# Performance work log

Measured on AMD Instinct MI355X. Metric: run time of the kernel, lower is better.

Reference implementation:

```python
import jax, jax.numpy as jnp
import numpy as np
import math

D = 256
N = 2048
B = 8
N_PLUS_1 = 2048  # masked index (1-based) in the score matrix


def setup_inputs() -> dict:
    key = jax.random.key(0)
    k1, k2, k3, k4, k5 = jax.random.split(key, 5)
    scale = 1.0 / math.sqrt(D)
    return {
        "Z_in": jax.random.normal(k1, (B, D + 1, N), dtype=jnp.float32),
        "A_l": jax.random.normal(k2, (D, D), dtype=jnp.float32) * scale,
        "r_l": jax.random.normal(k3, (1,), dtype=jnp.float32),
        "B_l": jax.random.normal(k4, (D, D), dtype=jnp.float32) * scale,
        "C_l": jax.random.normal(k5, (D, D), dtype=jnp.float32) * scale,
    }


def reference(Z_in, A_l, r_l, B_l, C_l):
    # Z_in: (B, d+1, N)
    X = Z_in[:, :D, :]   # (B, d, N)
    Y = Z_in[:, D:, :]   # (B, 1, N)
    U = jnp.einsum('ij,bjn->bin', B_l, X)  # (B, d, N)
    W = jnp.einsum('ij,bjn->bin', C_l, X)  # (B, d, N)
    scores = jnp.einsum('bdn,bdm->bnm', U, W)  # (B, N, N) = U^T W
    att = jax.nn.relu(scores)                  # h_type == 'relu'
    # zero the (n_plus_1-1, n_plus_1-1) diagonal entry of the attention core
    att = att.at[:, N_PLUS_1 - 1, N_PLUS_1 - 1].set(0.0)
    X_att = jnp.einsum('bdn,bnm->bdm', X, att)  # (B, d, N)
    X_out = X + jnp.einsum('ij,bjm->bim', A_l, X_att)
    Y_out = Y + r_l * jnp.einsum('bdn,bnm->bdm', Y, att)
    return jnp.concatenate([X_out, Y_out], axis=1)  # (B, d+1, N)
```

## Files before the change

kernel.cpp:

```cpp
#include <hip/hip_runtime.h>

#define D 256
#define N 2048
#define NB 8
#define ZSTRIDE (257 * 2048)

typedef __attribute__((ext_vector_type(8))) short short8;
typedef __attribute__((ext_vector_type(4))) short short4v;
typedef __attribute__((ext_vector_type(4))) float f32x4;

#define MFMA(a, b, c) __builtin_amdgcn_mfma_f32_16x16x32_bf16((a), (b), (c), 0, 0, 0)

#define GLOAD_LDS16(g, s) __builtin_amdgcn_global_load_lds( \
    (const __attribute__((address_space(1))) void*)(g),     \
    (__attribute__((address_space(3))) void*)(s), 16, 0, 0)

__device__ __forceinline__ short f2bf(float f) {
    unsigned u = __builtin_bit_cast(unsigned, f);
    u += 0x7fffu + ((u >> 16) & 1u);
    return (short)(u >> 16);
}
__device__ __forceinline__ float bf2f(short s) {
    unsigned u = ((unsigned)(unsigned short)s) << 16;
    return __builtin_bit_cast(float, u);
}

__global__ __launch_bounds__(256) void prep_small(
    const float* __restrict__ B_l, const float* __restrict__ C_l,
    const float* __restrict__ A_l, const float* __restrict__ Z,
    short* __restrict__ G, short* __restrict__ Ab, short* __restrict__ Yb)
{
    int blk = blockIdx.x, tid = threadIdx.x;
    if (blk < 256) {
        float s = 0.f;
        #pragma unroll 8
        for (int k = 0; k < 256; ++k)
            s += B_l[k * 256 + blk] * C_l[k * 256 + tid];
        G[blk * 256 + tid] = f2bf(s);
    } else if (blk < 320) {
        int base = (blk - 256) * 1024 + tid;
        #pragma unroll
        for (int r = 0; r < 4; ++r) {
            int idx = base + r * 256;
            Ab[idx] = f2bf(A_l[idx]);
        }
    } else {
        int base = (blk - 320) * 1024 + tid;
        #pragma unroll
        for (int r = 0; r < 4; ++r) {
            int idx = base + r * 256;
            int b = idx >> 11, n = idx & 2047;
            Yb[idx] = f2bf(Z[(size_t)b * ZSTRIDE + 256 * N + n]);
        }
    }
}

__global__ __launch_bounds__(256) void transpose_kernel(
    const float* __restrict__ Z, short* __restrict__ Xt)
{
    typedef __attribute__((ext_vector_type(4))) float f4;
    __shared__ short t[64][68];
    int blk = blockIdx.x;
    int b = blk & 7;
    int dt = (blk >> 3) & 3;
    int nt = blk >> 5;
    int d0 = dt * 64, n0 = nt * 64;
    const float* ZB = Z + (size_t)b * ZSTRIDE;
    int tid = threadIdx.x;
    #pragma unroll
    for (int k = 0; k < 4; ++k) {
        int f = tid + k * 256;
        int r = f >> 4, c4 = f & 15;
        f4 v = *(const f4*)(ZB + (size_t)(d0 + r) * N + n0 + c4 * 4);
        #pragma unroll
        for (int j = 0; j < 4; ++j) t[r][c4 * 4 + j] = f2bf(v[j]);
    }
    __syncthreads();
    short* XtB = Xt + (size_t)b * (N * D);
    #pragma unroll
    for (int k = 0; k < 2; ++k) {
        int f = tid + k * 256;
        int n = f >> 3, c8 = f & 7;
        short8 v;
        #pragma unroll
        for (int j = 0; j < 8; ++j) v[j] = t[c8 * 8 + j][n];
        *(short8*)(XtB + (size_t)(n0 + n) * D + d0 + c8 * 8) = v;
    }
}

__global__ __launch_bounds__(512, 4) void prep_gemm2(
    const short* __restrict__ Xt, const short* __restrict__ G,
    const short* __restrict__ Ab, short* __restrict__ Wt, short* __restrict__ Px)
{
    __shared__ __align__(16) char smem[65536];
    typedef short TileT[128][64];
    TileT* As = (TileT*)smem;
    TileT* Bs = (TileT*)(smem + 32768);

    int blk = blockIdx.x;
    int half = blk >> 8;
    int r0 = blk & 255;
    int b = r0 >> 5;
    int idx = r0 & 31;

    const short* Arows;
    const short* Brows;
    short* Cout;
    size_t cstride;
    int row_base, col_base;
    if (half == 0) {
        row_base = (idx & 15) << 7;
        col_base = (idx >> 4) << 7;
        Arows = Xt + (size_t)b * (N * D);
        Brows = G;
        Cout  = Wt + (size_t)b * (N * D);
        cstride = D;
    } else {
        row_base = (idx & 1) << 7;
        col_base = (idx >> 1) << 7;
        Arows = Ab;
        Brows = Xt + (size_t)b * (N * D);
        Cout  = Px + (size_t)b * (D * N);
        cstride = N;
    }

    int tid = threadIdx.x;
    int w = tid >> 6, l = tid & 63;
    int l16 = l & 15, lq = l >> 4;
    int wm = w >> 2, wn = w & 3;
    int lrow8 = l >> 3, lc = l & 7;

    auto STAGE = [&](const short* base, int row0g, int kt, TileT* dst) {
        #pragma unroll
        for (int i = 0; i < 2; ++i) {
            int rloc = i * 64 + w * 8;
            int row = rloc + lrow8;
            const char* src = (const char*)(base + (size_t)(row0g + row) * D)
                              + kt * 128 + ((lc ^ (row & 7)) * 16);
            GLOAD_LDS16(src, &(*dst)[rloc][0]);
        }
    };

    f32x4 zero4 = {0.f, 0.f, 0.f, 0.f};
    f32x4 acc[4][2];
    #pragma unroll
    for (int mi = 0; mi < 4; ++mi)
        #pragma unroll
        for (int ni = 0; ni < 2; ++ni) acc[mi][ni] = zero4;

    STAGE(Arows, row_base, 0, &As[0]);
    STAGE(Brows, col_base, 0, &Bs[0]);
    __syncthreads();

    int buf = 0;
    #pragma unroll
    for (int kt = 0; kt < 4; ++kt) {
        if (kt < 3) {
            STAGE(Arows, row_base, kt + 1, &As[buf ^ 1]);
            STAGE(Brows, col_base, kt + 1, &Bs[buf ^ 1]);
        }
        #pragma unroll
        for (int ks = 0; ks < 2; ++ks) {
            short8 af[4], bf[2];
            #pragma unroll
            for (int mi = 0; mi < 4; ++mi) {
                int r = wm * 64 + mi * 16 + l16;
                af[mi] = *(const short8*)(&As[buf][r][(ks * 32 + lq * 8) ^ ((r & 7) << 3)]);
            }
            #pragma unroll
            for (int ni = 0; ni < 2; ++ni) {
                int r = wn * 32 + ni * 16 + l16;
                bf[ni] = *(const short8*)(&Bs[buf][r][(ks * 32 + lq * 8) ^ ((r & 7) << 3)]);
            }
            #pragma unroll
            for (int mi = 0; mi < 4; ++mi)
                #pragma unroll
                for (int ni = 0; ni < 2; ++ni)
                    acc[mi][ni] = MFMA(af[mi], bf[ni], acc[mi][ni]);
        }
        __syncthreads();
        buf ^= 1;
    }

    short* cq = (short*)smem + (size_t)w * (64 * 40);
    #pragma unroll
    for (int mi = 0; mi < 4; ++mi)
        #pragma unroll
        for (int ni = 0; ni < 2; ++ni)
            #pragma unroll
            for (int rg = 0; rg < 4; ++rg)
                cq[(mi * 16 + lq * 4 + rg) * 40 + ni * 16 + l16] =
                    f2bf(acc[mi][ni][rg]);
    #pragma unroll
    for (int p = 0; p < 4; ++p) {
        int row = p * 16 + (l >> 2), c8 = l & 3;
        short8 v = *(const short8*)(&cq[row * 40 + c8 * 8]);
        *(short8*)(Cout + (size_t)(row_base + wm * 64 + row) * cstride +
                   col_base + wn * 32 + c8 * 8) = v;
    }
}

__global__ __launch_bounds__(512, 4) void scores_kernel(
    const short* __restrict__ Xt, const short* __restrict__ Wt,
    const short* __restrict__ Yb, short* __restrict__ attT,
    float* __restrict__ accY, int bBase, int nbMask, int nbShift)
{
    __shared__ __align__(16) char smem[65536];
    typedef short TileT[128][64];
    TileT* As = (TileT*)smem;
    TileT* Bs = (TileT*)(smem + 32768);

    int blk = blockIdx.x;
    int b_local = blk & nbMask;
    int idx = blk >> nbShift;
    int m_base = (idx & 15) << 7;
    int n_base = (idx >> 4) << 7;
    int b = bBase + b_local;

    int tid = threadIdx.x;
    int w = tid >> 6, l = tid & 63;
    int l16 = l & 15, lq = l >> 4;
    int wm = w >> 2, wn = w & 3;
    int lrow8 = l >> 3, lc = l & 7;

    const short* WtB = Wt + (size_t)b * (N * D);
    const short* XtB = Xt + (size_t)b * (N * D);
    const short* YbB = Yb + (size_t)b * N;
    float* accYB = accY + (size_t)b * N;
    short* attTB = attT + (size_t)b_local * N * N;

    auto STAGE = [&](const short* base, int row0g, int kt, TileT* dst) {
        #pragma unroll
        for (int i = 0; i < 2; ++i) {
            int rloc = i * 64 + w * 8;
            int row = rloc + lrow8;
            const char* src = (const char*)(base + (size_t)(row0g + row) * D)
                              + kt * 128 + ((lc ^ (row & 7)) * 16);
            GLOAD_LDS16(src, &(*dst)[rloc][0]);
        }
    };

    f32x4 zero4 = {0.f, 0.f, 0.f, 0.f};
    f32x4 acc[4][2];
    #pragma unroll
    for (int mi = 0; mi < 4; ++mi)
        #pragma unroll
        for (int ni = 0; ni < 2; ++ni) acc[mi][ni] = zero4;

    STAGE(WtB, m_base, 0, &As[0]);
    STAGE(XtB, n_base, 0, &Bs[0]);
    __syncthreads();

    int buf = 0;
    #pragma unroll
    for (int kt = 0; kt < 4; ++kt) {
        if (kt < 3) {
            STAGE(WtB, m_base, kt + 1, &As[buf ^ 1]);
            STAGE(XtB, n_base, kt + 1, &Bs[buf ^ 1]);
        }
        #pragma unroll
        for (int ks = 0; ks < 2; ++ks) {
            short8 af[4], bf[2];
            #pragma unroll
            for (int mi = 0; mi < 4; ++mi) {
                int r = wm * 64 + mi * 16 + l16;
                af[mi] = *(const short8*)(&As[buf][r][(ks * 32 + lq * 8) ^ ((r & 7) << 3)]);
            }
            #pragma unroll
            for (int ni = 0; ni < 2; ++ni) {
                int r = wn * 32 + ni * 16 + l16;
                bf[ni] = *(const short8*)(&Bs[buf][r][(ks * 32 + lq * 8) ^ ((r & 7) << 3)]);
            }
            #pragma unroll
            for (int mi = 0; mi < 4; ++mi)
                #pragma unroll
                for (int ni = 0; ni < 2; ++ni)
                    acc[mi][ni] = MFMA(af[mi], bf[ni], acc[mi][ni]);
        }
        __syncthreads();
        buf ^= 1;
    }

    bool corner = (m_base == 1920) && (n_base == 1920);
    #pragma unroll
    for (int mi = 0; mi < 4; ++mi)
        #pragma unroll
        for (int ni = 0; ni < 2; ++ni)
            #pragma unroll
            for (int rg = 0; rg < 4; ++rg) {
                float v = acc[mi][ni][rg];
                v = v > 0.f ? v : 0.f;
                if (corner) {
                    int gm = m_base + wm * 64 + mi * 16 + lq * 4 + rg;
                    int gn = n_base + wn * 32 + ni * 16 + l16;
                    if (gm == N - 1 && gn == N - 1) v = 0.f;
                }
                acc[mi][ni][rg] = v;
            }

    {
        float yv[2];
        #pragma unroll
        for (int ni = 0; ni < 2; ++ni)
            yv[ni] = bf2f(YbB[n_base + wn * 32 + ni * 16 + l16]);
        #pragma unroll
        for (int mi = 0; mi < 4; ++mi)
            #pragma unroll
            for (int rg = 0; rg < 4; ++rg) {
                float s = acc[mi][0][rg] * yv[0] + acc[mi][1][rg] * yv[1];
                s += __shfl_xor(s, 1);
                s += __shfl_xor(s, 2);
                s += __shfl_xor(s, 4);
                s += __shfl_xor(s, 8);
                if (l16 == 0)
                    atomicAdd(&accYB[m_base + wm * 64 + mi * 16 + lq * 4 + rg], s);
            }
    }

    {
        short* attq = (short*)smem + (size_t)w * (64 * 40);
        #pragma unroll
        for (int mi = 0; mi < 4; ++mi)
            #pragma unroll
            for (int ni = 0; ni < 2; ++ni)
                #pragma unroll
                for (int rg = 0; rg < 4; ++rg)
                    attq[(mi * 16 + lq * 4 + rg) * 40 + ni * 16 + l16] =
                        f2bf(acc[mi][ni][rg]);
        #pragma unroll
        for (int p = 0; p < 4; ++p) {
            int row = p * 16 + (l >> 2), c8 = l & 3;
            short8 v = *(const short8*)(&attq[row * 40 + c8 * 8]);
            *(short8*)(attTB + (size_t)(m_base + wm * 64 + row) * N +
                       n_base + wn * 32 + c8 * 8) = v;
        }
    }
}

__global__ __launch_bounds__(512, 4) void pv_kernel(
    const float* __restrict__ Z, const short* __restrict__ Px,
    const short* __restrict__ attT, float* __restrict__ out,
    int bBase, int nbMask, int nbShift)
{
    __shared__ __align__(16) char smem[49152];
    typedef short ATile[64][64];
    typedef short BTile[128][64];
    ATile* As = (ATile*)smem;
    BTile* Bs = (BTile*)(smem + 16384);

    int blk = blockIdx.x;
    int b_local = blk & nbMask;
    int idx = blk >> nbShift;
    int d_base = (idx & 3) << 6;
    int m_base = (idx >> 2) << 7;
    int b = bBase + b_local;

    int tid = threadIdx.x;
    int w = tid >> 6, l = tid & 63;
    int l16 = l & 15, lq = l >> 4;
    int wd = w >> 2, wm = w & 3;
    int lrow8 = l >> 3, lc = l & 7;

    const short* PxB = Px + (size_t)b * (D * N);
    const short* attTB = attT + (size_t)b_local * N * N;

    auto STAGE_A = [&](int kt, ATile* dst) {
        int rloc = w * 8;
        int row = rloc + lrow8;
        const char* src = (const char*)(PxB + (size_t)(d_base + row) * N)
                          + kt * 128 + ((lc ^ (row & 7)) * 16);
        GLOAD_LDS16(src, &(*dst)[rloc][0]);
    };
    auto STAGE_B = [&](int kt, BTile* dst) {
        #pragma unroll
        for (int i = 0; i < 2; ++i) {
            int rloc = i * 64 + w * 8;
            int row = rloc + lrow8;
            const char* src = (const char*)(attTB + (size_t)(m_base + row) * N)
                              + kt * 128 + ((lc ^ (row & 7)) * 16);
            GLOAD_LDS16(src, &(*dst)[rloc][0]);
        }
    };

    f32x4 zero4 = {0.f, 0.f, 0.f, 0.f};
    f32x4 acc[2][2];
    #pragma unroll
    for (int di = 0; di < 2; ++di)
        #pragma unroll
        for (int mj = 0; mj < 2; ++mj) acc[di][mj] = zero4;

    STAGE_A(0, &As[0]);
    STAGE_B(0, &Bs[0]);
    __syncthreads();

    int buf = 0;
    for (int kt = 0; kt < 32; ++kt) {
        if (kt < 31) {
            STAGE_A(kt + 1, &As[buf ^ 1]);
            STAGE_B(kt + 1, &Bs[buf ^ 1]);
        }
        #pragma unroll
        for (int ks = 0; ks < 2; ++ks) {
            short8 af[2], bf[2];
            #pragma unroll
            for (int di = 0; di < 2; ++di) {
                int r = wd * 32 + di * 16 + l16;
                af[di] = *(const short8*)(&As[buf][r][(ks * 32 + lq * 8) ^ ((r & 7) << 3)]);
            }
            #pragma unroll
            for (int mj = 0; mj < 2; ++mj) {
                int r = wm * 32 + mj * 16 + l16;
                bf[mj] = *(const short8*)(&Bs[buf][r][(ks * 32 + lq * 8) ^ ((r & 7) << 3)]);
            }
            #pragma unroll
            for (int di = 0; di < 2; ++di)
                #pragma unroll
                for (int mj = 0; mj < 2; ++mj)
                    acc[di][mj] = MFMA(af[di], bf[mj], acc[di][mj]);
        }
        __syncthreads();
        buf ^= 1;
    }

    #pragma unroll
    for (int di = 0; di < 2; ++di)
        #pragma unroll
        for (int mj = 0; mj < 2; ++mj)
            #pragma unroll
            for (int rg = 0; rg < 4; ++rg) {
                int dd = d_base + wd * 32 + di * 16 + lq * 4 + rg;
                int mm = m_base + wm * 32 + mj * 16 + l16;
                size_t off = (size_t)b * ZSTRIDE + (size_t)dd * N + mm;
                out[off] = Z[off] + acc[di][mj][rg];
            }
}

__global__ __launch_bounds__(256) void epilogue_y(
    const float* __restrict__ Z, const float* __restrict__ accY,
    const float* __restrict__ r_l, float* __restrict__ out)
{
    int i = blockIdx.x * 256 + threadIdx.x;
    int b = i >> 11, m = i & 2047;
    size_t off = (size_t)b * ZSTRIDE + (size_t)256 * N + m;
    out[off] = Z[off] + r_l[0] * accY[i];
}

__global__ __launch_bounds__(512, 4) void fused_kernel(
    const float* __restrict__ Z, const short* __restrict__ Xt,
    const short* __restrict__ Wt, const short* __restrict__ Px,
    const short* __restrict__ Yb, const float* __restrict__ r_l,
    float* __restrict__ out)
{
    __shared__ __align__(16) short xtsA[32][256];
    __shared__ __align__(16) short xtsB[32][256];
    __shared__ __align__(16) short attA[64][36];
    __shared__ __align__(16) short attB[64][36];

    int blk = blockIdx.x;
    int b = blk & 7;
    int m_base = (blk >> 3) << 6;
    int tid = threadIdx.x;
    int w = tid >> 6, l = tid & 63;
    int l16 = l & 15, lq = l >> 4;

    const short* XtB = Xt + (size_t)b * (N * D);
    const short* WtB = Wt + (size_t)b * (N * D);
    const short* PxB = Px + (size_t)b * (D * N);
    const short* YbB = Yb + b * N;

    int mi = w >> 1;
    int nj = w & 1;

    short8 a_wt[8];
    {
        const short* ap = WtB + (size_t)(m_base + 16 * mi + l16) * D + lq * 8;
        #pragma unroll
        for (int ks = 0; ks < 8; ++ks)
            a_wt[ks] = *(const short8*)(ap + ks * 32);
    }

    f32x4 zero4 = {0.f, 0.f, 0.f, 0.f};
    f32x4 accX[2][4];
    #pragma unroll
    for (int di = 0; di < 2; ++di)
        #pragma unroll
        for (int mj = 0; mj < 4; ++mj) accX[di][mj] = zero4;

    float accY = 0.f;
    int ym = tid >> 3, yseg = tid & 7;

    auto STAGE = [&](int it, short (*dst)[256]) {
        #pragma unroll
        for (int r = 0; r < 2; ++r) {
            int row  = r * 16 + 2 * w + (l >> 5);
            int colb = ((l & 31) * 16) ^ ((row & 7) << 4);
            const char* src = (const char*)(XtB + (size_t)(it * 32 + row) * D) + colb;
            GLOAD_LDS16(src, &dst[r * 16 + 2 * w][0]);
        }
    };

    auto BODY = [&](int it, short (*xrd)[256], short (*xst)[256], short (*atw)[36]) {
        int n_base = it * 32;
        if (it + 1 < 64) STAGE(it + 1, xst);
        short8 px[2];
        #pragma unroll
        for (int di = 0; di < 2; ++di)
            px[di] = *(const short8*)(PxB + (size_t)(32 * w + 16 * di + l16) * N +
                                      n_base + lq * 8);
        short4v yv = *(const short4v*)(YbB + n_base + yseg * 4);
        f32x4 sa = zero4;
        #pragma unroll
        for (int ks = 0; ks < 8; ++ks) {
            int colsh = (ks * 32 + lq * 8) ^ ((l16 & 7) << 3);
            short8 xb = *(const short8*)(&xrd[16 * nj + l16][colsh]);
            sa = MFMA(a_wt[ks], xb, sa);
        }
        {
            int nn = 16 * nj + l16;
            #pragma unroll
            for (int rg = 0; rg < 4; ++rg) {
                int mm = 16 * mi + lq * 4 + rg;
                float v = sa[rg] > 0.f ? sa[rg] : 0.f;
                if ((m_base + mm == N - 1) && (n_base + nn == N - 1)) v = 0.f;
                atw[mm][nn] = f2bf(v);
            }
        }
        __syncthreads();
        #pragma unroll
        for (int mj = 0; mj < 4; ++mj) {
            short8 bfr = *(const short8*)(&atw[16 * mj + l16][lq * 8]);
            #pragma unroll
            for (int di = 0; di < 2; ++di)
                accX[di][mj] = MFMA(px[di], bfr, accX[di][mj]);
        }
        {
            short4v av = *(const short4v*)(&atw[ym][yseg * 4]);
            #pragma unroll
            for (int j = 0; j < 4; ++j)
                accY += bf2f(av[j]) * bf2f(yv[j]);
        }
    };

    STAGE(0, xtsA);
    __syncthreads();
    for (int it2 = 0; it2 < 32; ++it2) {
        BODY(2 * it2,     xtsA, xtsB, attA);
        BODY(2 * it2 + 1, xtsB, xtsA, attB);
    }

    #pragma unroll
    for (int di = 0; di < 2; ++di)
        #pragma unroll
        for (int mj = 0; mj < 4; ++mj)
            #pragma unroll
            for (int rg = 0; rg < 4; ++rg) {
                int dd = 32 * w + 16 * di + lq * 4 + rg;
                int mm = m_base + 16 * mj + l16;
                size_t off = (size_t)b * ZSTRIDE + (size_t)dd * N + mm;
                out[off] = Z[off] + accX[di][mj][rg];
            }
    accY += __shfl_xor(accY, 1);
    accY += __shfl_xor(accY, 2);
    accY += __shfl_xor(accY, 4);
    if (yseg == 0) {
        float r = r_l[0];
        int mm = m_base + ym;
        size_t off = (size_t)b * ZSTRIDE + (size_t)256 * N + mm;
        out[off] = Z[off] + r * accY;
    }
}

extern "C" void kernel_launch(void* const* d_in, const int* in_sizes, int n_in,
                              void* d_out, int out_size, void* d_ws, size_t ws_size,
                              hipStream_t stream) {
    const float* Z   = (const float*)d_in[0];
    const float* A_l = (const float*)d_in[1];
    const float* r_l = (const float*)d_in[2];
    const float* B_l = (const float*)d_in[3];
    const float* C_l = (const float*)d_in[4];
    float* out = (float*)d_out;

    char* ws = (char*)d_ws;
    short* G    = (short*)(ws);
    short* Ab   = (short*)(ws + 131072);
    short* Xt   = (short*)(ws + 262144);
    short* Wt   = (short*)(ws + 8650752);
    short* Px   = (short*)(ws + 17039360);
    short* Yb   = (short*)(ws + 25427968);
    float* accY = (float*)(ws + 25460736);
    short* attT = (short*)(ws + 25526272);

    const size_t baseNeed = 25526272;
    const size_t attSz = (size_t)N * N * 2;
    int NBCH = 8, nbShift = 3;
    while (NBCH > 1 && baseNeed + (size_t)NBCH * attSz > ws_size) { NBCH >>= 1; --nbShift; }
    bool decomposed = (baseNeed + (size_t)NBCH * attSz <= ws_size);

    prep_small<<<336, 256, 0, stream>>>(B_l, C_l, A_l, Z, G, Ab, Yb);
    transpose_kernel<<<1024, 256, 0, stream>>>(Z, Xt);
    prep_gemm2<<<512, 512, 0, stream>>>(Xt, G, Ab, Wt, Px);

    if (decomposed) {
        hipMemsetAsync(accY, 0, NB * N * sizeof(float), stream);
        int nbMask = NBCH - 1;
        for (int c = 0; c < NB / NBCH; ++c) {
            int bBase = c * NBCH;
            scores_kernel<<<NBCH * 256, 512, 0, stream>>>(
                Xt, Wt, Yb, attT, accY, bBase, nbMask, nbShift);
            pv_kernel<<<NBCH * 64, 512, 0, stream>>>(
                Z, Px, attT, out, bBase, nbMask, nbShift);
        }
        epilogue_y<<<64, 256, 0, stream>>>(Z, accY, r_l, out);
    } else {
        fused_kernel<<<256, 512, 0, stream>>>(Z, Xt, Wt, Px, Yb, r_l, out);
    }
}
```

Measured before the change: 103.0 us.

## Keep Wt fragments in registers across eight N-tiles and enlarge pv tiles

The scores kernel now loads each wave's Wt row fragments into registers once, then loops over eight consecutive 128-column N tiles, streaming only Xt through double-buffered LDS and writing each output tile in turn. This removes the repeated staging of Wt and cuts the grid from 256 to 32 blocks per batch. The pv kernel doubles its M tile to 256, so each wave holds more accumulators and each A tile is reused across more columns. In exchange, register pressure rises (launch bounds relaxed to 2), LDS use grows, and fewer blocks may leave some CUs underoccupied.

```diff
diff --git a/kernel.cpp b/kernel.cpp
--- a/kernel.cpp
+++ b/kernel.cpp
@@ -200,21 +200,19 @@
     }
 }
 
-__global__ __launch_bounds__(512, 4) void scores_kernel(
+__global__ __launch_bounds__(512, 2) void scores_kernel(
     const short* __restrict__ Xt, const short* __restrict__ Wt,
     const short* __restrict__ Yb, short* __restrict__ attT,
     float* __restrict__ accY, int bBase, int nbMask, int nbShift)
 {
-    __shared__ __align__(16) char smem[65536];
-    typedef short TileT[128][64];
-    TileT* As = (TileT*)smem;
-    TileT* Bs = (TileT*)(smem + 32768);
+    __shared__ __align__(16) short Bs[2][128][64];
+    __shared__ __align__(16) short scratch[8][64][40];
 
     int blk = blockIdx.x;
     int b_local = blk & nbMask;
     int idx = blk >> nbShift;
     int m_base = (idx & 15) << 7;
-    int n_base = (idx >> 4) << 7;
+    int nsup = (idx >> 4) << 10;
     int b = bBase + b_local;
 
     int tid = threadIdx.x;
@@ -229,110 +227,123 @@
     float* accYB = accY + (size_t)b * N;
     short* attTB = attT + (size_t)b_local * N * N;
 
-    auto STAGE = [&](const short* base, int row0g, int kt, TileT* dst) {
+    short8 af[4][4][2];
+    #pragma unroll
+    for (int mi = 0; mi < 4; ++mi)
+        #pragma unroll
+        for (int kt = 0; kt < 4; ++kt)
+            #pragma unroll
+            for (int ks = 0; ks < 2; ++ks)
+                af[mi][kt][ks] = *(const short8*)(
+                    WtB + (size_t)(m_base + wm * 64 + mi * 16 + l16) * D +
+                    kt * 64 + ks * 32 + lq * 8);
+
+    f32x4 zero4 = {0.f, 0.f, 0.f, 0.f};
+    f32x4 acc[4][2];
+    #pragma unroll
+    for (int mi = 0; mi < 4; ++mi)
+        #pragma unroll
+        for (int ni = 0; ni < 2; ++ni) acc[mi][ni] = zero4;
+
+    auto STAGE_B = [&](int nb, int kt, int bufidx) {
         #pragma unroll
         for (int i = 0; i < 2; ++i) {
             int rloc = i * 64 + w * 8;
             int row = rloc + lrow8;
-            const char* src = (const char*)(base + (size_t)(row0g + row) * D)
+            const char* src = (const char*)(XtB + (size_t)(nb + row) * D)
                               + kt * 128 + ((lc ^ (row & 7)) * 16);
-            GLOAD_LDS16(src, &(*dst)[rloc][0]);
+            GLOAD_LDS16(src, &Bs[bufidx][rloc][0]);
         }
     };
 
-    f32x4 zero4 = {0.f, 0.f, 0.f, 0.f};
-    f32x4 acc[4][2];
-    #pragma unroll
-    for (int mi = 0; mi < 4; ++mi)
-        #pragma unroll
-        for (int ni = 0; ni < 2; ++ni) acc[mi][ni] = zero4;
-
-    STAGE(WtB, m_base, 0, &As[0]);
-    STAGE(XtB, n_base, 0, &Bs[0]);
+    STAGE_B(nsup, 0, 0);
     __syncthreads();
 
-    int buf = 0;
-    #pragma unroll
-    for (int kt = 0; kt < 4; ++kt) {
-        if (kt < 3) {
-            STAGE(WtB, m_base, kt + 1, &As[buf ^ 1]);
-            STAGE(XtB, n_base, kt + 1, &Bs[buf ^ 1]);
-        }
-        #pragma unroll
-        for (int ks = 0; ks < 2; ++ks) {
-            short8 af[4], bf[2];
-            #pragma unroll
-            for (int mi = 0; mi < 4; ++mi) {
-                int r = wm * 64 + mi * 16 + l16;
-                af[mi] = *(const short8*)(&As[buf][r][(ks * 32 + lq * 8) ^ ((r & 7) << 3)]);
-            }
-            #pragma unroll
-            for (int ni = 0; ni < 2; ++ni) {
-                int r = wn * 32 + ni * 16 + l16;
-                bf[ni] = *(const short8*)(&Bs[buf][r][(ks * 32 + lq * 8) ^ ((r & 7) << 3)]);
-            }
-            #pragma unroll
-            for (int mi = 0; mi < 4; ++mi)
+    for (int s = 0; s < 8; ++s) {
+        int n_base = nsup + s * 128;
+        #pragma unroll
+        for (int kt = 0; kt < 4; ++kt) {
+            if (kt < 3) {
+                STAGE_B(n_base, kt + 1, (kt + 1) & 1);
+            } else if (s < 7) {
+                STAGE_B(n_base + 128, 0, 0);
+            }
+
+            #pragma unroll
+            for (int ks = 0; ks < 2; ++ks) {
+                short8 bf[2];
                 #pragma unroll
-                for (int ni = 0; ni < 2; ++ni)
-                    acc[mi][ni] = MFMA(af[mi], bf[ni], acc[mi][ni]);
-        }
-        __syncthreads();
-        buf ^= 1;
-    }
-
-    bool corner = (m_base == 1920) && (n_base == 1920);
-    #pragma unroll
-    for (int mi = 0; mi < 4; ++mi)
-        #pragma unroll
-        for (int ni = 0; ni < 2; ++ni)
-            #pragma unroll
-            for (int rg = 0; rg < 4; ++rg) {
-                float v = acc[mi][ni][rg];
-                v = v > 0.f ? v : 0.f;
-                if (corner) {
-                    int gm = m_base + wm * 64 + mi * 16 + lq * 4 + rg;
-                    int gn = n_base + wn * 32 + ni * 16 + l16;
-                    if (gm == N - 1 && gn == N - 1) v = 0.f;
+                for (int ni = 0; ni < 2; ++ni) {
+                    int r = wn * 32 + ni * 16 + l16;
+                    bf[ni] = *(const short8*)(
+                        &Bs[kt & 1][r][(ks * 32 + lq * 8) ^ ((r & 7) << 3)]);
                 }
-                acc[mi][ni][rg] = v;
-            }
-
-    {
-        float yv[2];
-        #pragma unroll
-        for (int ni = 0; ni < 2; ++ni)
-            yv[ni] = bf2f(YbB[n_base + wn * 32 + ni * 16 + l16]);
-        #pragma unroll
-        for (int mi = 0; mi < 4; ++mi)
-            #pragma unroll
-            for (int rg = 0; rg < 4; ++rg) {
-                float s = acc[mi][0][rg] * yv[0] + acc[mi][1][rg] * yv[1];
-                s += __shfl_xor(s, 1);
-                s += __shfl_xor(s, 2);
-                s += __shfl_xor(s, 4);
-                s += __shfl_xor(s, 8);
-                if (l16 == 0)
-                    atomicAdd(&accYB[m_base + wm * 64 + mi * 16 + lq * 4 + rg], s);
-            }
-    }
-
-    {
-        short* attq = (short*)smem + (size_t)w * (64 * 40);
-        #pragma unroll
-        for (int mi = 0; mi < 4; ++mi)
-            #pragma unroll
-            for (int ni = 0; ni < 2; ++ni)
                 #pragma unroll
-                for (int rg = 0; rg < 4; ++rg)
-                    attq[(mi * 16 + lq * 4 + rg) * 40 + ni * 16 + l16] =
-                        f2bf(acc[mi][ni][rg]);
-        #pragma unroll
-        for (int p = 0; p < 4; ++p) {
-            int row = p * 16 + (l >> 2), c8 = l & 3;
-            short8 v = *(const short8*)(&attq[row * 40 + c8 * 8]);
-            *(short8*)(attTB + (size_t)(m_base + wm * 64 + row) * N +
-                       n_base + wn * 32 + c8 * 8) = v;
+                for (int mi = 0; mi < 4; ++mi)
+                    #pragma unroll
+                    for (int ni = 0; ni < 2; ++ni)
+                        acc[mi][ni] = MFMA(af[mi][kt][ks], bf[ni], acc[mi][ni]);
+            }
+
+            if (kt == 3) {
+                bool corner = (m_base == 1920) && (n_base == 1920);
+                #pragma unroll
+                for (int mi = 0; mi < 4; ++mi)
+                    #pragma unroll
+                    for (int ni = 0; ni < 2; ++ni)
+                        #pragma unroll
+                        for (int rg = 0; rg < 4; ++rg) {
+                            float v = acc[mi][ni][rg];
+                            v = v > 0.f ? v : 0.f;
+                            if (corner) {
+                                int gm = m_base + wm * 64 + mi * 16 + lq * 4 + rg;
+                                int gn = n_base + wn * 32 + ni * 16 + l16;
+                                if (gm == N - 1 && gn == N - 1) v = 0.f;
+                            }
+                            acc[mi][ni][rg] = v;
+                        }
+                {
+                    float yv[2];
+                    #pragma unroll
+                    for (int ni = 0; ni < 2; ++ni)
+                        yv[ni] = bf2f(YbB[n_base + wn * 32 + ni * 16 + l16]);
+                    #pragma unroll
+                    for (int mi = 0; mi < 4; ++mi)
+                        #pragma unroll
+                        for (int rg = 0; rg < 4; ++rg) {
+                            float sY = acc[mi][0][rg] * yv[0] + acc[mi][1][rg] * yv[1];
+                            sY += __shfl_xor(sY, 1);
+                            sY += __shfl_xor(sY, 2);
+                            sY += __shfl_xor(sY, 4);
+                            sY += __shfl_xor(sY, 8);
+                            if (l16 == 0)
+                                atomicAdd(&accYB[m_base + wm * 64 + mi * 16 + lq * 4 + rg], sY);
+                        }
+                }
+                {
+                    short* sq = &scratch[w][0][0];
+                    #pragma unroll
+                    for (int mi = 0; mi < 4; ++mi)
+                        #pragma unroll
+                        for (int ni = 0; ni < 2; ++ni)
+                            #pragma unroll
+                            for (int rg = 0; rg < 4; ++rg)
+                                sq[(mi * 16 + lq * 4 + rg) * 40 + ni * 16 + l16] =
+                                    f2bf(acc[mi][ni][rg]);
+                    #pragma unroll
+                    for (int p = 0; p < 4; ++p) {
+                        int row = p * 16 + (l >> 2), c8 = l & 3;
+                        short8 v = *(const short8*)(&sq[row * 40 + c8 * 8]);
+                        *(short8*)(attTB + (size_t)(m_base + wm * 64 + row) * N +
+                                   n_base + wn * 32 + c8 * 8) = v;
+                    }
+                }
+                #pragma unroll
+                for (int mi = 0; mi < 4; ++mi)
+                    #pragma unroll
+                    for (int ni = 0; ni < 2; ++ni) acc[mi][ni] = zero4;
+            }
+            __syncthreads();
         }
     }
 }
@@ -342,9 +353,9 @@
     const short* __restrict__ attT, float* __restrict__ out,
     int bBase, int nbMask, int nbShift)
 {
-    __shared__ __align__(16) char smem[49152];
+    __shared__ __align__(16) char smem[81920];
     typedef short ATile[64][64];
-    typedef short BTile[128][64];
+    typedef short BTile[256][64];
     ATile* As = (ATile*)smem;
     BTile* Bs = (BTile*)(smem + 16384);
 
@@ -352,7 +363,7 @@
     int b_local = blk & nbMask;
     int idx = blk >> nbShift;
     int d_base = (idx & 3) << 6;
-    int m_base = (idx >> 2) << 7;
+    int m_base = (idx >> 2) << 8;
     int b = bBase + b_local;
 
     int tid = threadIdx.x;
@@ -373,7 +384,7 @@
     };
     auto STAGE_B = [&](int kt, BTile* dst) {
         #pragma unroll
-        for (int i = 0; i < 2; ++i) {
+        for (int i = 0; i < 4; ++i) {
             int rloc = i * 64 + w * 8;
             int row = rloc + lrow8;
             const char* src = (const char*)(attTB + (size_t)(m_base + row) * N)
@@ -383,11 +394,11 @@
     };
 
     f32x4 zero4 = {0.f, 0.f, 0.f, 0.f};
-    f32x4 acc[2][2];
+    f32x4 acc[2][4];
     #pragma unroll
     for (int di = 0; di < 2; ++di)
         #pragma unroll
-        for (int mj = 0; mj < 2; ++mj) acc[di][mj] = zero4;
+        for (int mj = 0; mj < 4; ++mj) acc[di][mj] = zero4;
 
     STAGE_A(0, &As[0]);
     STAGE_B(0, &Bs[0]);
@@ -401,21 +412,21 @@
         }
         #pragma unroll
         for (int ks = 0; ks < 2; ++ks) {
-            short8 af[2], bf[2];
+            short8 af[2], bf[4];
             #pragma unroll
             for (int di = 0; di < 2; ++di) {
                 int r = wd * 32 + di * 16 + l16;
                 af[di] = *(const short8*)(&As[buf][r][(ks * 32 + lq * 8) ^ ((r & 7) << 3)]);
             }
             #pragma unroll
-            for (int mj = 0; mj < 2; ++mj) {
-                int r = wm * 32 + mj * 16 + l16;
+            for (int mj = 0; mj < 4; ++mj) {
+                int r = wm * 64 + mj * 16 + l16;
                 bf[mj] = *(const short8*)(&Bs[buf][r][(ks * 32 + lq * 8) ^ ((r & 7) << 3)]);
             }
             #pragma unroll
             for (int di = 0; di < 2; ++di)
                 #pragma unroll
-                for (int mj = 0; mj < 2; ++mj)
+                for (int mj = 0; mj < 4; ++mj)
                     acc[di][mj] = MFMA(af[di], bf[mj], acc[di][mj]);
         }
         __syncthreads();
@@ -425,11 +436,11 @@
     #pragma unroll
     for (int di = 0; di < 2; ++di)
         #pragma unroll
-        for (int mj = 0; mj < 2; ++mj)
+        for (int mj = 0; mj < 4; ++mj)
             #pragma unroll
             for (int rg = 0; rg < 4; ++rg) {
                 int dd = d_base + wd * 32 + di * 16 + lq * 4 + rg;
-                int mm = m_base + wm * 32 + mj * 16 + l16;
+                int mm = m_base + wm * 64 + mj * 16 + l16;
                 size_t off = (size_t)b * ZSTRIDE + (size_t)dd * N + mm;
                 out[off] = Z[off] + acc[di][mj][rg];
             }
@@ -605,9 +616,9 @@
         int nbMask = NBCH - 1;
         for (int c = 0; c < NB / NBCH; ++c) {
             int bBase = c * NBCH;
-            scores_kernel<<<NBCH * 256, 512, 0, stream>>>(
+            scores_kernel<<<NBCH * 32, 512, 0, stream>>>(
                 Xt, Wt, Yb, attT, accY, bBase, nbMask, nbShift);
-            pv_kernel<<<NBCH * 64, 512, 0, stream>>>(
+            pv_kernel<<<NBCH * 32, 512, 0, stream>>>(
                 Z, Px, attT, out, bBase, nbMask, nbShift);
         }
         epilogue_y<<<64, 256, 0, stream>>>(Z, accY, r_l, out);
```

Result: slower. 120.1 us (+16.6%).

## Enlarge scores kernel tile to 128x256 with 32-wide K steps

Applied to the files above, without the earlier changes.

Changes the scores GEMM tile from 128x128 to 128x256 per block, so each wave computes 64x64 instead of 64x32. The K tile shrinks from 64 to 32 and the loop now runs 8 stages, with a new XOR swizzle for the narrower rows. The goal is more MFMA reuse per LDS fragment load and half as many blocks reloading the shared W rows. In exchange it uses more accumulator registers and synchronizes more often, and the grid halves, which lowers parallelism.

```diff
diff --git a/kernel.cpp b/kernel.cpp
--- a/kernel.cpp
+++ b/kernel.cpp
@@ -205,23 +205,24 @@
     const short* __restrict__ Yb, short* __restrict__ attT,
     float* __restrict__ accY, int bBase, int nbMask, int nbShift)
 {
-    __shared__ __align__(16) char smem[65536];
-    typedef short TileT[128][64];
-    TileT* As = (TileT*)smem;
-    TileT* Bs = (TileT*)(smem + 32768);
+    __shared__ __align__(16) char smem[49152];
+    typedef short ATile[128][32];
+    typedef short BTile[256][32];
+    ATile* As = (ATile*)smem;
+    BTile* Bs = (BTile*)(smem + 16384);
 
     int blk = blockIdx.x;
     int b_local = blk & nbMask;
     int idx = blk >> nbShift;
     int m_base = (idx & 15) << 7;
-    int n_base = (idx >> 4) << 7;
+    int n_base = (idx >> 4) << 8;
     int b = bBase + b_local;
 
     int tid = threadIdx.x;
     int w = tid >> 6, l = tid & 63;
     int l16 = l & 15, lq = l >> 4;
     int wm = w >> 2, wn = w & 3;
-    int lrow8 = l >> 3, lc = l & 7;
+    int lr4 = l >> 2, lc4 = l & 3;
 
     const short* WtB = Wt + (size_t)b * (N * D);
     const short* XtB = Xt + (size_t)b * (N * D);
@@ -229,85 +230,86 @@
     float* accYB = accY + (size_t)b * N;
     short* attTB = attT + (size_t)b_local * N * N;
 
-    auto STAGE = [&](const short* base, int row0g, int kt, TileT* dst) {
+    auto STAGE_A = [&](int kt, int bi) {
+        int row = w * 16 + lr4;
+        const char* src = (const char*)(WtB + (size_t)(m_base + row) * D)
+                          + kt * 64 + ((lc4 ^ ((row >> 1) & 3)) * 16);
+        GLOAD_LDS16(src, &As[bi][w * 16][0]);
+    };
+    auto STAGE_B = [&](int kt, int bi) {
         #pragma unroll
         for (int i = 0; i < 2; ++i) {
-            int rloc = i * 64 + w * 8;
-            int row = rloc + lrow8;
-            const char* src = (const char*)(base + (size_t)(row0g + row) * D)
-                              + kt * 128 + ((lc ^ (row & 7)) * 16);
-            GLOAD_LDS16(src, &(*dst)[rloc][0]);
+            int row = i * 128 + w * 16 + lr4;
+            const char* src = (const char*)(XtB + (size_t)(n_base + row) * D)
+                              + kt * 64 + ((lc4 ^ ((row >> 1) & 3)) * 16);
+            GLOAD_LDS16(src, &Bs[bi][i * 128 + w * 16][0]);
         }
     };
 
     f32x4 zero4 = {0.f, 0.f, 0.f, 0.f};
-    f32x4 acc[4][2];
+    f32x4 acc[4][4];
     #pragma unroll
     for (int mi = 0; mi < 4; ++mi)
         #pragma unroll
-        for (int ni = 0; ni < 2; ++ni) acc[mi][ni] = zero4;
-
-    STAGE(WtB, m_base, 0, &As[0]);
-    STAGE(XtB, n_base, 0, &Bs[0]);
+        for (int ni = 0; ni < 4; ++ni) acc[mi][ni] = zero4;
+
+    STAGE_A(0, 0);
+    STAGE_B(0, 0);
     __syncthreads();
 
-    int buf = 0;
-    #pragma unroll
-    for (int kt = 0; kt < 4; ++kt) {
-        if (kt < 3) {
-            STAGE(WtB, m_base, kt + 1, &As[buf ^ 1]);
-            STAGE(XtB, n_base, kt + 1, &Bs[buf ^ 1]);
-        }
-        #pragma unroll
-        for (int ks = 0; ks < 2; ++ks) {
-            short8 af[4], bf[2];
-            #pragma unroll
-            for (int mi = 0; mi < 4; ++mi) {
-                int r = wm * 64 + mi * 16 + l16;
-                af[mi] = *(const short8*)(&As[buf][r][(ks * 32 + lq * 8) ^ ((r & 7) << 3)]);
-            }
-            #pragma unroll
-            for (int ni = 0; ni < 2; ++ni) {
-                int r = wn * 32 + ni * 16 + l16;
-                bf[ni] = *(const short8*)(&Bs[buf][r][(ks * 32 + lq * 8) ^ ((r & 7) << 3)]);
-            }
-            #pragma unroll
-            for (int mi = 0; mi < 4; ++mi)
-                #pragma unroll
-                for (int ni = 0; ni < 2; ++ni)
-                    acc[mi][ni] = MFMA(af[mi], bf[ni], acc[mi][ni]);
-        }
+    #pragma unroll
+    for (int kt = 0; kt < 8; ++kt) {
+        if (kt < 7) {
+            STAGE_A(kt + 1, (kt + 1) & 1);
+            STAGE_B(kt + 1, (kt + 1) & 1);
+        }
+        short8 af[4], bf[4];
+        #pragma unroll
+        for (int mi = 0; mi < 4; ++mi) {
+            int r = wm * 64 + mi * 16 + l16;
+            af[mi] = *(const short8*)(&As[kt & 1][r][(lq ^ ((r >> 1) & 3)) * 8]);
+        }
+        #pragma unroll
+        for (int ni = 0; ni < 4; ++ni) {
+            int r = wn * 64 + ni * 16 + l16;
+            bf[ni] = *(const short8*)(&Bs[kt & 1][r][(lq ^ ((r >> 1) & 3)) * 8]);
+        }
+        #pragma unroll
+        for (int mi = 0; mi < 4; ++mi)
+            #pragma unroll
+            for (int ni = 0; ni < 4; ++ni)
+                acc[mi][ni] = MFMA(af[mi], bf[ni], acc[mi][ni]);
         __syncthreads();
-        buf ^= 1;
-    }
-
-    bool corner = (m_base == 1920) && (n_base == 1920);
+    }
+
+    bool corner = (m_base == 1920) && (n_base == 1792);
     #pragma unroll
     for (int mi = 0; mi < 4; ++mi)
         #pragma unroll
-        for (int ni = 0; ni < 2; ++ni)
+        for (int ni = 0; ni < 4; ++ni)
             #pragma unroll
             for (int rg = 0; rg < 4; ++rg) {
                 float v = acc[mi][ni][rg];
                 v = v > 0.f ? v : 0.f;
                 if (corner) {
                     int gm = m_base + wm * 64 + mi * 16 + lq * 4 + rg;
-                    int gn = n_base + wn * 32 + ni * 16 + l16;
+                    int gn = n_base + wn * 64 + ni * 16 + l16;
                     if (gm == N - 1 && gn == N - 1) v = 0.f;
                 }
                 acc[mi][ni][rg] = v;
             }
 
     {
-        float yv[2];
-        #pragma unroll
-        for (int ni = 0; ni < 2; ++ni)
-            yv[ni] = bf2f(YbB[n_base + wn * 32 + ni * 16 + l16]);
+        float yv[4];
+        #pragma unroll
+        for (int ni = 0; ni < 4; ++ni)
+            yv[ni] = bf2f(YbB[n_base + wn * 64 + ni * 16 + l16]);
         #pragma unroll
         for (int mi = 0; mi < 4; ++mi)
             #pragma unroll
             for (int rg = 0; rg < 4; ++rg) {
-                float s = acc[mi][0][rg] * yv[0] + acc[mi][1][rg] * yv[1];
+                float s = acc[mi][0][rg] * yv[0] + acc[mi][1][rg] * yv[1]
+                        + acc[mi][2][rg] * yv[2] + acc[mi][3][rg] * yv[3];
                 s += __shfl_xor(s, 1);
                 s += __shfl_xor(s, 2);
                 s += __shfl_xor(s, 4);
@@ -318,21 +320,24 @@
     }
 
     {
-        short* attq = (short*)smem + (size_t)w * (64 * 40);
-        #pragma unroll
-        for (int mi = 0; mi < 4; ++mi)
-            #pragma unroll
-            for (int ni = 0; ni < 2; ++ni)
+        short* sq = (short*)smem + (size_t)w * (64 * 40);
+        #pragma unroll
+        for (int h = 0; h < 2; ++h) {
+            #pragma unroll
+            for (int mi = 0; mi < 4; ++mi)
                 #pragma unroll
-                for (int rg = 0; rg < 4; ++rg)
-                    attq[(mi * 16 + lq * 4 + rg) * 40 + ni * 16 + l16] =
-                        f2bf(acc[mi][ni][rg]);
-        #pragma unroll
-        for (int p = 0; p < 4; ++p) {
-            int row = p * 16 + (l >> 2), c8 = l & 3;
-            short8 v = *(const short8*)(&attq[row * 40 + c8 * 8]);
-            *(short8*)(attTB + (size_t)(m_base + wm * 64 + row) * N +
-                       n_base + wn * 32 + c8 * 8) = v;
+                for (int nih = 0; nih < 2; ++nih)
+                    #pragma unroll
+                    for (int rg = 0; rg < 4; ++rg)
+                        sq[(mi * 16 + lq * 4 + rg) * 40 + nih * 16 + l16] =
+                            f2bf(acc[mi][h * 2 + nih][rg]);
+            #pragma unroll
+            for (int p = 0; p < 4; ++p) {
+                int row = p * 16 + lr4, c8 = lc4;
+                short8 v = *(const short8*)(&sq[row * 40 + c8 * 8]);
+                *(short8*)(attTB + (size_t)(m_base + wm * 64 + row) * N +
+                           n_base + wn * 64 + h * 32 + c8 * 8) = v;
+            }
         }
     }
 }
@@ -605,7 +610,7 @@
         int nbMask = NBCH - 1;
         for (int c = 0; c < NB / NBCH; ++c) {
             int bBase = c * NBCH;
-            scores_kernel<<<NBCH * 256, 512, 0, stream>>>(
+            scores_kernel<<<NBCH * 128, 512, 0, stream>>>(
                 Xt, Wt, Yb, attT, accY, bBase, nbMask, nbShift);
             pv_kernel<<<NBCH * 64, 512, 0, stream>>>(
                 Z, Px, attT, out, bBase, nbMask, nbShift);
```

Result: faster. 99.21 us (-3.6%).
